# Kernel optimization log

Hardware: AMD Instinct MI355X
Metric: run time of the kernel (lower is better)

Reference implementation:

```python
import jax, jax.numpy as jnp
import numpy as np

RATIO = 0.95
EPS = 1e-8
BIDIRECTIONAL = True


def _normalize_desc(fmap):
    # fmap: [1, ch, h, w] -> [h*w, ch], L2-normalized rows
    ch = fmap.shape[1]
    d = fmap.reshape(ch, -1).T
    return d / jnp.sqrt(jnp.sum(jnp.square(d), axis=1, keepdims=True))


def setup_inputs() -> dict:
    key = jax.random.key(0)
    k1, k2 = jax.random.split(key)
    map_A = jax.random.normal(k1, (1, 512, 96, 128), dtype=jnp.float32)
    map_B = jax.random.normal(k2, (1, 512, 96, 128), dtype=jnp.float32)
    return {"map_A": map_A, "map_B": map_B}


def reference(map_A, map_B):
    d1 = _normalize_desc(map_A)  # [N1, ch]
    d2 = _normalize_desc(map_B)  # [N2, ch]

    sim = d1 @ d2.T  # [N1, N2]

    # A -> B: top-2 over columns
    nns_sim12, nns12 = jax.lax.top_k(sim, 2)
    nns_dist12 = 2.0 - 2.0 * nns_sim12
    ratios12 = nns_dist12[:, 0] / (nns_dist12[:, 1] + EPS)
    nn12 = nns12[:, 0]
    match_sim = nns_sim12[:, 0]

    # B -> A: top-2 over rows of sim (columns of sim.T)
    nns_sim21, nns21 = jax.lax.top_k(sim.T, 2)
    nns_dist21 = 2.0 - 2.0 * nns_sim21
    ratios21 = nns_dist21[:, 0] / (nns_dist21[:, 1] + EPS)
    nn21 = nns21[:, 0]
    if not BIDIRECTIONAL:
        ratios21 = ratios21 * 0.0

    ids1 = jnp.arange(sim.shape[0])
    mask = (ids1 == nn21[nn12]) & (ratios12 <= RATIO) & (ratios21[nn12] <= RATIO)

    masked_sim = jnp.where(mask, match_sim, 0.0)
    return masked_sim, nn12, mask
```

## Files before the change

### kernel.cpp

```cpp
#include <hip/hip_runtime.h>
#include <stdint.h>

#define N      12288
#define CH     512
#define NTILE  96
#define NS     8
#define JT_PER_S 12

typedef _Float16 f16x8 __attribute__((ext_vector_type(8)));
typedef float    f32x4 __attribute__((ext_vector_type(4)));

struct Top2 { float v0, v1; int i0, i1; };

__device__ float g_invA[N];
__device__ float g_invB[N];
__device__ unsigned short g_AT[(size_t)N * 1024];
__device__ unsigned short g_BT[(size_t)N * 1024];
__device__ Top2  g_rpart[NS][N];
__device__ Top2  g_cpart[NTILE][N];
__device__ int   g_nn12[N];
__device__ float g_r12[N];
__device__ float g_sim0[N];
__device__ int   g_nn21[N];
__device__ float g_r21[N];

__device__ __forceinline__ void t2_ins(float v, int idx,
                                       float& v0, int& i0, float& v1, int& i1) {
  bool beats0 = (v > v0) || (v == v0 && idx < i0);
  bool beats1 = (v > v1) || (v == v1 && idx < i1);
  if (beats0) { v1 = v0; i1 = i0; v0 = v; i0 = idx; }
  else if (beats1) { v1 = v; i1 = idx; }
}

__device__ __forceinline__ float bf16_quant(float f) {
  unsigned int u = __float_as_uint(f);
  unsigned int r = 0x7fffu + ((u >> 16) & 1u);
  unsigned int q = ((u + r) >> 16) << 16;
  return __uint_as_float(q);
}

__device__ __forceinline__ void gload16(const void* g, void* lds) {
  __builtin_amdgcn_global_load_lds((const __attribute__((address_space(1))) void*)g,
                                   (__attribute__((address_space(3))) void*)lds,
                                   16, 0, 0);
}

__global__ __launch_bounds__(256)
void prep_kernel(const float* __restrict__ A, const float* __restrict__ B) {
  const int d0 = blockIdx.x * 64;
  const float* src = blockIdx.y ? B : A;
  unsigned short* dst = blockIdx.y ? g_BT : g_AT;
  float* inv = blockIdx.y ? g_invB : g_invA;

  __shared__ float Ls[32][68];
  __shared__ unsigned short Os[64][64];
  __shared__ float Ps[4][64];

  const int t = threadIdx.x;
  const int a = t >> 6, dl = t & 63;
  float sum = 0.f;

  for (int g = 0; g < 16; ++g) {
    __syncthreads();
    {
      const int c = t >> 3, dc = (t & 7) * 8;
      const float* p = src + (size_t)(g * 32 + c) * N + d0 + dc;
      float4 v0 = *reinterpret_cast<const float4*>(p);
      float4 v1 = *reinterpret_cast<const float4*>(p + 4);
      *reinterpret_cast<float4*>(&Ls[c][dc])     = v0;
      *reinterpret_cast<float4*>(&Ls[c][dc + 4]) = v1;
    }
    __syncthreads();
    {
      _Float16 hv[8] __attribute__((aligned(16)));
      _Float16 lv[8] __attribute__((aligned(16)));
#pragma unroll
      for (int j = 0; j < 8; ++j) {
        float v = Ls[a * 8 + j][dl] * 1024.0f;
        sum += v * v;
        _Float16 h = (_Float16)v;
        float rr = v - (float)h;
        hv[j] = h;
        lv[j] = (_Float16)rr;
      }
      *reinterpret_cast<uint4*>(&Os[dl][a * 8])      = *reinterpret_cast<const uint4*>(hv);
      *reinterpret_cast<uint4*>(&Os[dl][32 + a * 8]) = *reinterpret_cast<const uint4*>(lv);
    }
    __syncthreads();
    {
#pragma unroll
      for (int p2 = 0; p2 < 2; ++p2) {
        const int d = p2 * 32 + (t >> 3), ch = t & 7;
        const int sc = ch ^ (d & 7);
        *reinterpret_cast<uint4*>((char*)(dst + (size_t)(d0 + d) * 1024) + g * 128 + sc * 16)
            = *reinterpret_cast<const uint4*>(&Os[d][ch * 8]);
      }
    }
  }
  Ps[a][dl] = sum;
  __syncthreads();
  if (t < 64) {
    float tot = Ps[0][t] + Ps[1][t] + Ps[2][t] + Ps[3][t];
    inv[d0 + t] = 1.0f / sqrtf(tot);
  }
}

__global__ __launch_bounds__(256, 3)
void sim_top2_mfma() {
  __shared__ unsigned short As[128 * 64];
  __shared__ unsigned short Bs[128 * 64];
  __shared__ Top2 rowW[2][128];
  __shared__ Top2 colW[2][128];
  __shared__ float iaS[128];
  __shared__ float ibS[128];

  const int itile = blockIdx.x, slice = blockIdx.y;
  const int i0 = itile * 128;
  const int tid = threadIdx.x;
  const int wave = tid >> 6, lane = tid & 63;
  const int wr = wave >> 1, wc = wave & 1;
  const int fr = lane & 15, kq = lane >> 4;

  if (tid < 128) {
    iaS[tid] = g_invA[i0 + tid];
    Top2 z; z.v0 = -1e30f; z.v1 = -1e30f; z.i0 = 0x7fffffff; z.i1 = 0x7fffffff;
    rowW[0][tid] = z; rowW[1][tid] = z;
  }

  const char* gAl = (const char*)g_AT
      + (size_t)(i0 + wave * 32 + (lane >> 3)) * 2048 + (lane & 7) * 16;
  char* const ldsA0 = (char*)As + wave * 4096;
  char* const ldsB0 = (char*)Bs + wave * 4096;

  const int f7 = fr & 7;
  const int cHi = (kq ^ f7) << 4;
  const int cLo = ((kq + 4) ^ f7) << 4;
  int aOff[4], bOff[4];
#pragma unroll
  for (int mi = 0; mi < 4; ++mi) aOff[mi] = (wr * 64 + mi * 16 + fr) * 128;
#pragma unroll
  for (int ni = 0; ni < 4; ++ni) bOff[ni] = (wc * 64 + ni * 16 + fr) * 128;

  for (int jt = slice * JT_PER_S; jt < slice * JT_PER_S + JT_PER_S; ++jt) {
    const int j0 = jt * 128;
    if (tid < 128) ibS[tid] = g_invB[j0 + tid];

    f32x4 acc[4][4];
#pragma unroll
    for (int mi = 0; mi < 4; ++mi)
#pragma unroll
      for (int ni = 0; ni < 4; ++ni)
#pragma unroll
        for (int q = 0; q < 4; ++q) acc[mi][ni][q] = 0.f;

    const char* gBl = (const char*)g_BT
        + (size_t)(j0 + wave * 32 + (lane >> 3)) * 2048 + (lane & 7) * 16;

    for (int g = 0; g < 16; ++g) {
      __syncthreads();
#pragma unroll
      for (int it = 0; it < 4; ++it) {
        gload16(gAl + (size_t)it * 8 * 2048 + (size_t)g * 128, ldsA0 + it * 1024);
        gload16(gBl + (size_t)it * 8 * 2048 + (size_t)g * 128, ldsB0 + it * 1024);
      }
      __syncthreads();

      f16x8 ah[4], al[4];
#pragma unroll
      for (int mi = 0; mi < 4; ++mi) {
        ah[mi] = *reinterpret_cast<const f16x8*>((const char*)As + aOff[mi] + cHi);
        al[mi] = *reinterpret_cast<const f16x8*>((const char*)As + aOff[mi] + cLo);
      }
#pragma unroll
      for (int ni = 0; ni < 4; ++ni) {
        f16x8 bh = *reinterpret_cast<const f16x8*>((const char*)Bs + bOff[ni] + cHi);
        f16x8 bl = *reinterpret_cast<const f16x8*>((const char*)Bs + bOff[ni] + cLo);
#pragma unroll
        for (int mi = 0; mi < 4; ++mi) {
          acc[mi][ni] = __builtin_amdgcn_mfma_f32_16x16x32_f16(ah[mi], bh, acc[mi][ni], 0, 0, 0);
          acc[mi][ni] = __builtin_amdgcn_mfma_f32_16x16x32_f16(ah[mi], bl, acc[mi][ni], 0, 0, 0);
          acc[mi][ni] = __builtin_amdgcn_mfma_f32_16x16x32_f16(al[mi], bh, acc[mi][ni], 0, 0, 0);
        }
      }
    }

    float ib[4];
#pragma unroll
    for (int ni = 0; ni < 4; ++ni) ib[ni] = ibS[wc * 64 + ni * 16 + fr];
#pragma unroll
    for (int mi = 0; mi < 4; ++mi)
#pragma unroll
      for (int r = 0; r < 4; ++r) {
        const float iar = iaS[wr * 64 + mi * 16 + kq * 4 + r];
#pragma unroll
        for (int ni = 0; ni < 4; ++ni)
          acc[mi][ni][r] *= iar * ib[ni];
      }

#pragma unroll
    for (int mi = 0; mi < 4; ++mi) {
#pragma unroll
      for (int r = 0; r < 4; ++r) {
        const int row = wr * 64 + mi * 16 + kq * 4 + r;
        float v0 = -1e30f, v1 = -1e30f; int id0 = 0x7fffffff, id1 = 0x7fffffff;
#pragma unroll
        for (int ni = 0; ni < 4; ++ni)
          t2_ins(acc[mi][ni][r], j0 + wc * 64 + ni * 16 + fr, v0, id0, v1, id1);
#pragma unroll
        for (int m = 1; m < 16; m <<= 1) {
          float ov0 = __shfl_xor(v0, m), ov1 = __shfl_xor(v1, m);
          int oi0 = __shfl_xor(id0, m), oi1 = __shfl_xor(id1, m);
          t2_ins(ov0, oi0, v0, id0, v1, id1);
          t2_ins(ov1, oi1, v0, id0, v1, id1);
        }
        if (fr == 0) {
          Top2 tT = rowW[wc][row];
          t2_ins(v0, id0, tT.v0, tT.i0, tT.v1, tT.i1);
          t2_ins(v1, id1, tT.v0, tT.i0, tT.v1, tT.i1);
          rowW[wc][row] = tT;
        }
      }
    }

#pragma unroll
    for (int ni = 0; ni < 4; ++ni) {
      float v0 = -1e30f, v1 = -1e30f; int id0 = 0x7fffffff, id1 = 0x7fffffff;
#pragma unroll
      for (int mi = 0; mi < 4; ++mi)
#pragma unroll
        for (int r = 0; r < 4; ++r)
          t2_ins(acc[mi][ni][r], i0 + wr * 64 + mi * 16 + kq * 4 + r, v0, id0, v1, id1);
#pragma unroll
      for (int m = 16; m < 64; m <<= 1) {
        float ov0 = __shfl_xor(v0, m), ov1 = __shfl_xor(v1, m);
        int oi0 = __shfl_xor(id0, m), oi1 = __shfl_xor(id1, m);
        t2_ins(ov0, oi0, v0, id0, v1, id1);
        t2_ins(ov1, oi1, v0, id0, v1, id1);
      }
      if (kq == 0) {
        Top2 tT; tT.v0 = v0; tT.v1 = v1; tT.i0 = id0; tT.i1 = id1;
        colW[wr][wc * 64 + ni * 16 + fr] = tT;
      }
    }
    __syncthreads();
    if (tid < 128) {
      Top2 tT = colW[0][tid];
      Top2 o  = colW[1][tid];
      t2_ins(o.v0, o.i0, tT.v0, tT.i0, tT.v1, tT.i1);
      t2_ins(o.v1, o.i1, tT.v0, tT.i0, tT.v1, tT.i1);
      g_cpart[itile][j0 + tid] = tT;
    }
  }

  __syncthreads();
  if (tid < 128) {
    Top2 tT = rowW[0][tid];
    Top2 o  = rowW[1][tid];
    t2_ins(o.v0, o.i0, tT.v0, tT.i0, tT.v1, tT.i1);
    t2_ins(o.v1, o.i1, tT.v0, tT.i0, tT.v1, tT.i1);
    g_rpart[slice][i0 + tid] = tT;
  }
}

__global__ void merge_kernel() {
  int i = blockIdx.x * 256 + threadIdx.x;
  if (i >= N) return;
  {
    float v0 = -1e30f, v1 = -1e30f; int id0 = 0x7fffffff, id1 = 0x7fffffff;
#pragma unroll
    for (int s = 0; s < NS; ++s) {
      Top2 p = g_rpart[s][i];
      t2_ins(p.v0, p.i0, v0, id0, v1, id1);
      t2_ins(p.v1, p.i1, v0, id0, v1, id1);
    }
    float d0 = 2.f - 2.f * v0, d1 = 2.f - 2.f * v1;
    g_nn12[i] = id0; g_r12[i] = d0 / (d1 + 1e-8f); g_sim0[i] = v0;
  }
  {
    float v0 = -1e30f, v1 = -1e30f; int id0 = 0x7fffffff, id1 = 0x7fffffff;
    for (int it = 0; it < NTILE; ++it) {
      Top2 p = g_cpart[it][i];
      t2_ins(p.v0, p.i0, v0, id0, v1, id1);
      t2_ins(p.v1, p.i1, v0, id0, v1, id1);
    }
    float d0 = 2.f - 2.f * v0, d1 = 2.f - 2.f * v1;
    g_nn21[i] = id0; g_r21[i] = d0 / (d1 + 1e-8f);
  }
}

__global__ void finalize_kernel(float* __restrict__ out) {
  int i = blockIdx.x * 256 + threadIdx.x;
  if (i >= N) return;
  int j = g_nn12[i];
  int jc = j < 0 ? 0 : (j >= N ? N - 1 : j);
  bool mask = (g_nn21[jc] == i) && (g_r12[i] <= 0.95f) && (g_r21[jc] <= 0.95f);
  out[i]         = bf16_quant(mask ? g_sim0[i] : 0.f);
  out[N + i]     = bf16_quant((float)j);
  out[2 * N + i] = mask ? 1.f : 0.f;
}

extern "C" void kernel_launch(void* const* d_in, const int* in_sizes, int n_in,
                              void* d_out, int out_size, void* d_ws, size_t ws_size,
                              hipStream_t stream) {
  const float* A = (const float*)d_in[0];
  const float* B = (const float*)d_in[1];
  (void)d_ws; (void)ws_size;

  prep_kernel<<<dim3(192, 2), 256, 0, stream>>>(A, B);
  sim_top2_mfma<<<dim3(NTILE, NS), 256, 0, stream>>>();
  merge_kernel<<<dim3((N + 255) / 256), 256, 0, stream>>>();
  finalize_kernel<<<dim3((N + 255) / 256), 256, 0, stream>>>((float*)d_out);
}
```

Before: 2.333 ms.

## Double-buffer LDS tiles to overlap global loads with MFMA compute

Splits the shared-memory A/B tiles into two ping-pong buffers and issues the next k-chunk's global-to-LDS loads before computing on the current one, with one barrier per step instead of two. The first chunk of the next column tile is also prefetched before the epilogue. This targets load latency exposed between MFMA bursts. LDS use doubles, so launch bounds drop from 3 to 2 blocks per CU, which lowers occupancy. The manual vmcnt wait plus barrier ordering also risks races with epilogue LDS use.

```diff
diff --git a/kernel.cpp b/kernel.cpp
--- a/kernel.cpp
+++ b/kernel.cpp
@@ -105,10 +105,9 @@
   }
 }
 
-__global__ __launch_bounds__(256, 3)
+__global__ __launch_bounds__(256, 2)
 void sim_top2_mfma() {
-  __shared__ unsigned short As[128 * 64];
-  __shared__ unsigned short Bs[128 * 64];
+  __shared__ unsigned short SM[2][2][128 * 64];
   __shared__ Top2 rowW[2][128];
   __shared__ Top2 colW[2][128];
   __shared__ float iaS[128];
@@ -121,16 +120,33 @@
   const int wr = wave >> 1, wc = wave & 1;
   const int fr = lane & 15, kq = lane >> 4;
 
+  const char* gAl = (const char*)g_AT
+      + (size_t)(i0 + wave * 32 + (lane >> 3)) * 2048 + (lane & 7) * 16;
+
+  const int jtb = slice * JT_PER_S, jte = jtb + JT_PER_S;
+  const char* gBl = (const char*)g_BT
+      + (size_t)(jtb * 128 + wave * 32 + (lane >> 3)) * 2048 + (lane & 7) * 16;
+
+  auto stage = [&](int pp, int g_) {
+    char* la = (char*)&SM[pp][0][0] + wave * 4096;
+    char* lb = (char*)&SM[pp][1][0] + wave * 4096;
+    const char* ga = gAl + (size_t)g_ * 128;
+    const char* gb = gBl + (size_t)g_ * 128;
+#pragma unroll
+    for (int it = 0; it < 4; ++it) {
+      gload16(ga + (size_t)it * 8 * 2048, la + it * 1024);
+      gload16(gb + (size_t)it * 8 * 2048, lb + it * 1024);
+    }
+  };
+
+  stage(0, 0);
+
   if (tid < 128) {
     iaS[tid] = g_invA[i0 + tid];
     Top2 z; z.v0 = -1e30f; z.v1 = -1e30f; z.i0 = 0x7fffffff; z.i1 = 0x7fffffff;
     rowW[0][tid] = z; rowW[1][tid] = z;
   }
-
-  const char* gAl = (const char*)g_AT
-      + (size_t)(i0 + wave * 32 + (lane >> 3)) * 2048 + (lane & 7) * 16;
-  char* const ldsA0 = (char*)As + wave * 4096;
-  char* const ldsB0 = (char*)Bs + wave * 4096;
+  __syncthreads();
 
   const int f7 = fr & 7;
   const int cHi = (kq ^ f7) << 4;
@@ -141,7 +157,9 @@
 #pragma unroll
   for (int ni = 0; ni < 4; ++ni) bOff[ni] = (wc * 64 + ni * 16 + fr) * 128;
 
-  for (int jt = slice * JT_PER_S; jt < slice * JT_PER_S + JT_PER_S; ++jt) {
+  int p = 0;
+
+  for (int jt = jtb; jt < jte; ++jt) {
     const int j0 = jt * 128;
     if (tid < 128) ibS[tid] = g_invB[j0 + tid];
 
@@ -153,28 +171,24 @@
 #pragma unroll
         for (int q = 0; q < 4; ++q) acc[mi][ni][q] = 0.f;
 
-    const char* gBl = (const char*)g_BT
-        + (size_t)(j0 + wave * 32 + (lane >> 3)) * 2048 + (lane & 7) * 16;
-
     for (int g = 0; g < 16; ++g) {
-      __syncthreads();
-#pragma unroll
-      for (int it = 0; it < 4; ++it) {
-        gload16(gAl + (size_t)it * 8 * 2048 + (size_t)g * 128, ldsA0 + it * 1024);
-        gload16(gBl + (size_t)it * 8 * 2048 + (size_t)g * 128, ldsB0 + it * 1024);
-      }
-      __syncthreads();
-
+      asm volatile("s_waitcnt vmcnt(0)" ::: "memory");
+      __builtin_amdgcn_s_barrier();
+      asm volatile("" ::: "memory");
+      if (g < 15) stage(p ^ 1, g + 1);
+
+      const char* bA = (const char*)&SM[p][0][0];
+      const char* bB = (const char*)&SM[p][1][0];
       f16x8 ah[4], al[4];
 #pragma unroll
       for (int mi = 0; mi < 4; ++mi) {
-        ah[mi] = *reinterpret_cast<const f16x8*>((const char*)As + aOff[mi] + cHi);
-        al[mi] = *reinterpret_cast<const f16x8*>((const char*)As + aOff[mi] + cLo);
+        ah[mi] = *reinterpret_cast<const f16x8*>(bA + aOff[mi] + cHi);
+        al[mi] = *reinterpret_cast<const f16x8*>(bA + aOff[mi] + cLo);
       }
 #pragma unroll
       for (int ni = 0; ni < 4; ++ni) {
-        f16x8 bh = *reinterpret_cast<const f16x8*>((const char*)Bs + bOff[ni] + cHi);
-        f16x8 bl = *reinterpret_cast<const f16x8*>((const char*)Bs + bOff[ni] + cLo);
+        f16x8 bh = *reinterpret_cast<const f16x8*>(bB + bOff[ni] + cHi);
+        f16x8 bl = *reinterpret_cast<const f16x8*>(bB + bOff[ni] + cLo);
 #pragma unroll
         for (int mi = 0; mi < 4; ++mi) {
           acc[mi][ni] = __builtin_amdgcn_mfma_f32_16x16x32_f16(ah[mi], bh, acc[mi][ni], 0, 0, 0);
@@ -182,6 +196,13 @@
           acc[mi][ni] = __builtin_amdgcn_mfma_f32_16x16x32_f16(al[mi], bh, acc[mi][ni], 0, 0, 0);
         }
       }
+      asm volatile("" ::: "memory");
+      p ^= 1;
+    }
+    if (jt + 1 < jte) {
+      gBl = (const char*)g_BT
+          + (size_t)((jt + 1) * 128 + wave * 32 + (lane >> 3)) * 2048 + (lane & 7) * 16;
+      stage(p, 0);
     }
 
     float ib[4];
```

Measured after the change: 3.589 ms. 1.54x slower.
